# Optimization experiments

Measured on AMD Instinct MI355X. Metric: run time of the kernel, lower is better.

The kernel has to match this reference:

```python
import jax, jax.numpy as jnp
import numpy as np

N_UP, N_DOWN, N_NUC = 16, 16, 4
N_ELEC = N_UP + N_DOWN          # 32
N_ALL = N_ELEC + N_NUC          # 36
BASIS = 32
KDIM = 128                      # kernel_dim
EDIM = 128                      # embedding_dim
HID_K = 64                      # round(sqrt(32*128)) log-spaced hidden of kernel MLP
HID_O = 128                     # round(sqrt(128*128)) hidden of embed_out MLP
N_INT = 3
BATCH = 512
LOG2 = float(np.log(2.0))


def ssp(x):
    # shifted softplus used by SchNet: softplus(x) - log(2)
    return jax.nn.softplus(x) - LOG2


def _conv_indexing(n_elec, n_all):
    # np.mask_indices(n_all, nondiag): all off-diagonal (i, j), row-major
    mask = ~np.eye(n_all, dtype=bool)
    i, j = np.nonzero(mask)
    n = n_elec * (n_all - 1)
    return i[:n], j[:n]


def setup_inputs() -> dict:
    key = jax.random.key(0)
    ks = jax.random.split(key, 16)
    f32 = jnp.float32
    # per-spin shared electron embeddings (torch expand semantics)
    e_up = jax.random.normal(ks[0], (EDIM,), f32)
    e_down = jax.random.normal(ks[1], (EDIM,), f32)
    embedding_elec = jnp.concatenate(
        [jnp.tile(e_up, (N_UP, 1)), jnp.tile(e_down, (N_DOWN, 1))], axis=0
    )  # (N_ELEC, EDIM)
    embedding_nuc = jax.random.normal(ks[2], (N_NUC, KDIM), f32)

    def lin_init(k, out_d, in_d):
        bound = 1.0 / np.sqrt(in_d)
        return jax.random.uniform(k, (out_d, in_d), f32, -bound, bound)

    kk = jax.random.split(ks[3], 9 * N_INT)
    kernel_w1 = jnp.stack([lin_init(kk[9 * t + 0], HID_K, BASIS) for t in range(N_INT)])
    kernel_b1 = jnp.stack([jax.random.uniform(kk[9 * t + 1], (HID_K,), f32, -1, 1) * (1.0 / np.sqrt(BASIS)) for t in range(N_INT)])
    kernel_w2 = jnp.stack([lin_init(kk[9 * t + 2], KDIM, HID_K) for t in range(N_INT)])
    kernel_b2 = jnp.stack([jax.random.uniform(kk[9 * t + 3], (KDIM,), f32, -1, 1) * (1.0 / np.sqrt(HID_K)) for t in range(N_INT)])
    embed_in_w = jnp.stack([lin_init(kk[9 * t + 4], KDIM, EDIM) for t in range(N_INT)])
    embed_out_w1 = jnp.stack([lin_init(kk[9 * t + 5], HID_O, KDIM) for t in range(N_INT)])
    embed_out_b1 = jnp.stack([jax.random.uniform(kk[9 * t + 6], (HID_O,), f32, -1, 1) * (1.0 / np.sqrt(KDIM)) for t in range(N_INT)])
    embed_out_w2 = jnp.stack([lin_init(kk[9 * t + 7], EDIM, HID_O) for t in range(N_INT)])
    embed_out_b2 = jnp.stack([jax.random.uniform(kk[9 * t + 8], (EDIM,), f32, -1, 1) * (1.0 / np.sqrt(HID_O)) for t in range(N_INT)])

    dists_basis = jax.random.normal(ks[4], (BATCH, N_ELEC, N_ALL, BASIS), f32)
    return {
        "dists_basis": dists_basis,
        "embedding_elec": embedding_elec,
        "embedding_nuc": embedding_nuc,
        "kernel_w1": kernel_w1, "kernel_b1": kernel_b1,
        "kernel_w2": kernel_w2, "kernel_b2": kernel_b2,
        "embed_in_w": embed_in_w,
        "embed_out_w1": embed_out_w1, "embed_out_b1": embed_out_b1,
        "embed_out_w2": embed_out_w2, "embed_out_b2": embed_out_b2,
    }


def reference(dists_basis, embedding_elec, embedding_nuc,
              kernel_w1, kernel_b1, kernel_w2, kernel_b2,
              embed_in_w, embed_out_w1, embed_out_b1,
              embed_out_w2, embed_out_b2):
    B, n_elec, n_all, _ = dists_basis.shape
    c_i, c_j = _conv_indexing(n_elec, n_all)  # static numpy index arrays
    db = dists_basis[:, c_i, c_j, :]          # (B, n_pairs, BASIS)

    xs = jnp.broadcast_to(embedding_elec, (B, n_elec, EDIM))
    nuc = jnp.broadcast_to(embedding_nuc, (B, N_NUC, KDIM))
    for t in range(N_INT):
        # pairwise kernel MLP: BASIS -> HID_K -> KDIM with SSP
        h = ssp(jnp.einsum('bpi,hi->bph', db, kernel_w1[t]) + kernel_b1[t])
        Ws = jnp.einsum('bph,kh->bpk', h, kernel_w2[t]) + kernel_b2[t]  # (B,P,K)
        zs = jnp.einsum('bed,kd->bek', xs, embed_in_w[t])               # (B,n_elec,K)
        zs = jnp.concatenate([zs, nuc], axis=1)                         # (B,n_all,K)
        zj = zs[:, c_j]                                                 # (B,P,K)
        z = (Ws.reshape(B, n_elec, n_all - 1, KDIM)
             * zj.reshape(B, n_elec, n_all - 1, KDIM)).sum(axis=2)      # (B,n_elec,K)
        h2 = ssp(jnp.einsum('bek,hk->beh', z, embed_out_w1[t]) + embed_out_b1[t])
        xs = xs + jnp.einsum('beh,dh->bed', h2, embed_out_w2[t]) + embed_out_b2[t]
    return xs
```

## Files before the change

kernel.cpp:

```cpp
#include <hip/hip_runtime.h>
#include <hip/hip_bf16.h>
#include <stdint.h>

#define NBATCH 512
#define NE 32
#define NA 36
#define BAS 32
#define KD 128
#define ED 128
#define HK 64
#define HO 128
#define NT 3

#define XST 132
#define AST 136
#define ZJST 36
#define HB2 44

typedef uint16_t u16;
typedef uint32_t u32;
using bfrag = __attribute__((ext_vector_type(8))) short;
using f32x4 = __attribute__((ext_vector_type(4))) float;
using u32x2 = __attribute__((ext_vector_type(2))) unsigned int;
using u32x4 = __attribute__((ext_vector_type(4))) unsigned int;

#define MFMA(a, b, c) __builtin_amdgcn_mfma_f32_16x16x32_bf16(a, b, c, 0, 0, 0)

__device__ __forceinline__ short ftob(float f) {
    union { __hip_bfloat16 h; short s; } u;
    u.h = __float2bfloat16(f);
    return u.s;
}
__device__ __forceinline__ u32 pk2(float lo, float hi) {
    return ((u32)(u16)ftob(hi) << 16) | (u32)(u16)ftob(lo);
}
__device__ __forceinline__ float bf2f(u16 u) {
    return __uint_as_float(((u32)u) << 16);
}
__device__ __forceinline__ bfrag cvt8(float4 a, float4 c) {
    bfrag r;
    r[0] = ftob(a.x); r[1] = ftob(a.y); r[2] = ftob(a.z); r[3] = ftob(a.w);
    r[4] = ftob(c.x); r[5] = ftob(c.y); r[6] = ftob(c.z); r[7] = ftob(c.w);
    return r;
}
__device__ __forceinline__ bfrag ldf_frag(const float* p) {
    float4 a = *(const float4*)p;
    float4 c = *(const float4*)(p + 4);
    return cvt8(a, c);
}
__device__ __forceinline__ float sspv(float x) {
    return __logf(fmaf(__expf(x), 0.5f, 0.5f));
}

__global__ __launch_bounds__(512, 4) void schnet_mfma(
    const float* __restrict__ db_g,
    const float* __restrict__ ee_g,
    const float* __restrict__ en_g,
    const float* __restrict__ w1_g,
    const float* __restrict__ b1_g,
    const float* __restrict__ w2_g,
    const float* __restrict__ b2_g,
    const float* __restrict__ win_g,
    const float* __restrict__ wo1_g,
    const float* __restrict__ bo1_g,
    const float* __restrict__ wo2_g,
    const float* __restrict__ bo2_g,
    float* __restrict__ out_g)
{
    __shared__ __align__(16) float xs[NE * XST];
    __shared__ __align__(16) u16 xz[NE * AST];
    __shared__ __align__(16) u16 zst[KD * ZJST];
    __shared__ __align__(16) u32 arena32[8 * 16 * HB2];
    __shared__ __align__(16) u16 w2x[8 * 2 * 64 * 8];
    __shared__ __align__(16) u16 w1x[4 * 64 * 8];
    __shared__ __align__(16) float bb2[KD];
    __shared__ __align__(16) float sall[KD];
    __shared__ __align__(16) float bb1[HK];
    u16* h2b = (u16*)arena32;

    const int tid = threadIdx.x;
    const int b = blockIdx.x;
    const int w = tid >> 6;
    const int l = tid & 63;
    const int lm = l & 15;
    const int lq = l >> 4;

    {
        int idx = tid * 8;
        float4 v0 = *(const float4*)(ee_g + idx);
        float4 v1 = *(const float4*)(ee_g + idx + 4);
        int row = idx >> 7, col = idx & 127;
        *(float4*)&xs[row * XST + col] = v0;
        *(float4*)&xs[row * XST + col + 4] = v1;
        *(bfrag*)&xz[row * AST + col] = cvt8(v0, v1);
    }
    {
        int k = tid & 127, rr = tid >> 7;
        zst[k * ZJST + 32 + rr] = (u16)ftob(en_g[rr * 128 + k]);
    }
    __syncthreads();

    for (int t = 0; t < NT; t++) {
#pragma unroll
        for (int uu = 0; uu < 2; uu++) {
            int u = tid + uu * 512;
            int n = u >> 7, s = (u >> 6) & 1, lane = u & 63;
            int lmm = lane & 15, lqq = lane >> 4;
            const float* p = w2_g + (size_t)(t * KD + n * 16 + lmm) * HK + s * 32 + lqq * 8;
            *(bfrag*)&w2x[u * 8] = ldf_frag(p);
        }
        if (tid < 256) {
            int n = tid >> 6, lane = tid & 63;
            const float* p = w1_g + (size_t)(t * HK + n * 16 + (lane & 15)) * BAS
                             + ((lane >> 4) & 3) * 8;
            *(bfrag*)&w1x[tid * 8] = ldf_frag(p);
        } else if (tid < 384) {
            bb2[tid - 256] = b2_g[t * KD + tid - 256];
        } else if (tid < 448) {
            bb1[tid - 384] = b1_g[t * HK + tid - 384];
        }

        {
            bfrag wb[4];
#pragma unroll
            for (int ks = 0; ks < 4; ks++)
                wb[ks] = ldf_frag(win_g + (size_t)(t * KD + w * 16 + lm) * ED + ks * 32 + lq * 8);
            f32x4 c[2];
            c[0] = (f32x4){0.f, 0.f, 0.f, 0.f};
            c[1] = (f32x4){0.f, 0.f, 0.f, 0.f};
#pragma unroll
            for (int m = 0; m < 2; m++)
#pragma unroll
                for (int ks = 0; ks < 4; ks++) {
                    bfrag a = *(const bfrag*)&xz[(m * 16 + lm) * AST + ks * 32 + lq * 8];
                    c[m] = MFMA(a, wb[ks], c[m]);
                }
            u32x2 dd0, dd1;
            dd0.x = pk2(c[0][0], c[0][1]);
            dd0.y = pk2(c[0][2], c[0][3]);
            dd1.x = pk2(c[1][0], c[1][1]);
            dd1.y = pk2(c[1][2], c[1][3]);
            *(u32x2*)&zst[(w * 16 + lm) * ZJST + lq * 4] = dd0;
            *(u32x2*)&zst[(w * 16 + lm) * ZJST + 16 + lq * 4] = dd1;
            float s = __uint_as_float(dd0.x << 16) + __uint_as_float(dd0.x & 0xffff0000u)
                    + __uint_as_float(dd0.y << 16) + __uint_as_float(dd0.y & 0xffff0000u)
                    + __uint_as_float(dd1.x << 16) + __uint_as_float(dd1.x & 0xffff0000u)
                    + __uint_as_float(dd1.y << 16) + __uint_as_float(dd1.y & 0xffff0000u);
            s += __shfl_xor(s, 16, 64);
            s += __shfl_xor(s, 32, 64);
            u32x2 nd = *(const u32x2*)&zst[(w * 16 + lm) * ZJST + 32];
            s += __uint_as_float(nd.x << 16) + __uint_as_float(nd.x & 0xffff0000u)
               + __uint_as_float(nd.y << 16) + __uint_as_float(nd.y & 0xffff0000u);
            if (lq == 0) sall[w * 16 + lm] = s;
        }
        __syncthreads();

        {
            u32* hbw = arena32 + w * (16 * HB2);
            float4 a0, a1, b0, b1;
            const f32x4 zq = (f32x4){0.f, 0.f, 0.f, 0.f};

            auto tile_g12 = [&](bfrag ad, int jc, u32 kmA, u32 kmB, u32 kmC,
                                u32 kmD, float* acc) {
                f32x4 c1[4];
#pragma unroll
                for (int n = 0; n < 4; n++) {
                    f32x4 ci = *(const f32x4*)&bb1[n * 16 + lq * 4];
                    bfrag w1f = *(const bfrag*)&w1x[(n * 64 + l) * 8];
                    c1[n] = MFMA(w1f, ad, ci);
                }
#pragma unroll
                for (int n = 0; n < 4; n++) {
                    u32x2 pp;
                    pp.x = pk2(sspv(c1[n][0]), sspv(c1[n][1]));
                    pp.y = pk2(sspv(c1[n][2]), sspv(c1[n][3]));
                    *(u32x2*)&hbw[lm * HB2 + n * 8 + lq * 2] = pp;
                }
                __builtin_amdgcn_sched_barrier(0);
                union { u32x4 u; bfrag f; } ua, ub;
                ua.u = *(const u32x4*)&hbw[lm * HB2 + lq * 4];
                ub.u = *(const u32x4*)&hbw[lm * HB2 + 16 + lq * 4];
                bfrag a20 = ua.f;
                bfrag a21 = ub.f;
                __builtin_amdgcn_sched_barrier(0);
#pragma unroll
                for (int g = 0; g < 2; g++) {
#pragma unroll
                    for (int nn = 0; nn < 4; nn++) {
                        const int n = g * 4 + nn;
                        bfrag wf0 = *(const bfrag*)&w2x[(n * 128 + l) * 8];
                        bfrag wf1 = *(const bfrag*)&w2x[(n * 128 + 64 + l) * 8];
                        f32x4 c2 = MFMA(a20, wf0, zq);
                        c2 = MFMA(a21, wf1, c2);
                        u32x2 zd = *(const u32x2*)&zst[(n * 16 + lm) * ZJST + jc];
                        acc[n] = fmaf(c2[0], __uint_as_float((zd.x << 16) & kmA), acc[n]);
                        acc[n] = fmaf(c2[1], __uint_as_float(zd.x & kmB), acc[n]);
                        acc[n] = fmaf(c2[2], __uint_as_float((zd.y << 16) & kmC), acc[n]);
                        acc[n] = fmaf(c2[3], __uint_as_float(zd.y & kmD), acc[n]);
                    }
                    __builtin_amdgcn_sched_barrier(0);
                }
            };

            {
                {
                    int e0 = w * 4 + (lm >> 2), j0 = 32 + (lm & 3);
                    const float* p = db_g + ((size_t)(b * NE + e0) * NA + j0) * BAS + lq * 8;
                    a0 = *(const float4*)p;
                    a1 = *(const float4*)(p + 4);
                }
                {
                    const float* p = db_g + ((size_t)(b * NE + w * 4) * NA + lm) * BAS + lq * 8;
                    b0 = *(const float4*)p;
                    b1 = *(const float4*)(p + 4);
                }
                float znuc[8] = {0.f, 0.f, 0.f, 0.f, 0.f, 0.f, 0.f, 0.f};
                tile_g12(cvt8(a0, a1), 32, ~0u, 0xFFFF0000u, ~0u, 0xFFFF0000u, znuc);
                int e0 = w * 4 + lq;
#pragma unroll
                for (int n = 0; n < 8; n += 2) {
                    u32 pk = pk2(znuc[n], znuc[n + 1]);
                    xz[e0 * AST + n * 16 + lm] = (u16)pk;
                    xz[e0 * AST + (n + 1) * 16 + lm] = (u16)(pk >> 16);
                }
            }

#pragma unroll 1
            for (int le = 0; le < 4; le++) {
                const int e = w * 4 + le;
                float zreg[8] = {0.f, 0.f, 0.f, 0.f, 0.f, 0.f, 0.f, 0.f};
                {
                    const float* p = db_g + ((size_t)(b * NE + e) * NA + 16 + lm) * BAS + lq * 8;
                    a0 = *(const float4*)p;
                    a1 = *(const float4*)(p + 4);
                }
                {
                    int lp0 = lq * 4;
                    u32 k0 = (lp0 + 0 == e) ? 0u : ~0u;
                    u32 k1 = (lp0 + 1 == e) ? 0u : ~0u;
                    u32 k2 = (lp0 + 2 == e) ? 0u : ~0u;
                    u32 k3 = (lp0 + 3 == e) ? 0u : ~0u;
                    tile_g12(cvt8(b0, b1), lp0, k0, k1 & 0xFFFF0000u,
                             k2, k3 & 0xFFFF0000u, zreg);
                }
                {
                    int nle = (le < 3) ? le + 1 : 3;
                    const float* p = db_g + ((size_t)(b * NE + w * 4 + nle) * NA + lm) * BAS + lq * 8;
                    b0 = *(const float4*)p;
                    b1 = *(const float4*)(p + 4);
                }
                {
                    int lp0 = 16 + lq * 4;
                    u32 k0 = (lp0 + 0 == e) ? 0u : ~0u;
                    u32 k1 = (lp0 + 1 == e) ? 0u : ~0u;
                    u32 k2 = (lp0 + 2 == e) ? 0u : ~0u;
                    u32 k3 = (lp0 + 3 == e) ? 0u : ~0u;
                    tile_g12(cvt8(a0, a1), lp0, k0, k1 & 0xFFFF0000u,
                             k2, k3 & 0xFFFF0000u, zreg);
                }
#pragma unroll
                for (int n = 0; n < 8; n++) {
                    float v = zreg[n];
                    v += __shfl_xor(v, 16, 64);
                    v += __shfl_xor(v, 32, 64);
                    zreg[n] = v;
                }
                if (lq == le) {
#pragma unroll
                    for (int n = 0; n < 8; n += 2) {
                        int k0 = n * 16 + lm, k1 = (n + 1) * 16 + lm;
                        float o0 = bf2f(xz[e * AST + k0]);
                        float o1 = bf2f(xz[e * AST + k1]);
                        float ze0 = bf2f(zst[k0 * ZJST + e]);
                        float ze1 = bf2f(zst[k1 * ZJST + e]);
                        float t0 = zreg[n] + o0 + bb2[k0] * (sall[k0] - ze0);
                        float t1 = zreg[n + 1] + o1 + bb2[k1] * (sall[k1] - ze1);
                        u32 pk = pk2(t0, t1);
                        xz[e * AST + k0] = (u16)pk;
                        xz[e * AST + k1] = (u16)(pk >> 16);
                    }
                }
            }
        }
        __syncthreads();

        {
            bfrag wb[4];
#pragma unroll
            for (int ks = 0; ks < 4; ks++)
                wb[ks] = ldf_frag(wo1_g + (size_t)(t * HO + w * 16 + lm) * KD + ks * 32 + lq * 8);
            float bo1v = bo1_g[t * HO + w * 16 + lm];
            f32x4 c[2];
            c[0] = (f32x4){bo1v, bo1v, bo1v, bo1v};
            c[1] = (f32x4){bo1v, bo1v, bo1v, bo1v};
#pragma unroll
            for (int m = 0; m < 2; m++)
#pragma unroll
                for (int ks = 0; ks < 4; ks++) {
                    bfrag a = *(const bfrag*)&xz[(m * 16 + lm) * AST + ks * 32 + lq * 8];
                    c[m] = MFMA(a, wb[ks], c[m]);
                }
#pragma unroll
            for (int m = 0; m < 2; m++) {
                u32 p01 = pk2(sspv(c[m][0]), sspv(c[m][1]));
                u32 p23 = pk2(sspv(c[m][2]), sspv(c[m][3]));
                h2b[(m * 16 + lq * 4 + 0) * AST + w * 16 + lm] = (u16)p01;
                h2b[(m * 16 + lq * 4 + 1) * AST + w * 16 + lm] = (u16)(p01 >> 16);
                h2b[(m * 16 + lq * 4 + 2) * AST + w * 16 + lm] = (u16)p23;
                h2b[(m * 16 + lq * 4 + 3) * AST + w * 16 + lm] = (u16)(p23 >> 16);
            }
        }
        __syncthreads();

        {
            bfrag wb[4];
#pragma unroll
            for (int ks = 0; ks < 4; ks++)
                wb[ks] = ldf_frag(wo2_g + (size_t)(t * ED + w * 16 + lm) * HO + ks * 32 + lq * 8);
            float bo2v = bo2_g[t * ED + w * 16 + lm];
            f32x4 c[2];
            c[0] = (f32x4){bo2v, bo2v, bo2v, bo2v};
            c[1] = (f32x4){bo2v, bo2v, bo2v, bo2v};
#pragma unroll
            for (int m = 0; m < 2; m++)
#pragma unroll
                for (int ks = 0; ks < 4; ks++) {
                    bfrag a = *(const bfrag*)&h2b[(m * 16 + lm) * AST + ks * 32 + lq * 8];
                    c[m] = MFMA(a, wb[ks], c[m]);
                }
#pragma unroll
            for (int m = 0; m < 2; m++) {
                float nv[4];
#pragma unroll
                for (int r = 0; r < 4; r++) {
                    int row = m * 16 + lq * 4 + r, col = w * 16 + lm;
                    nv[r] = xs[row * XST + col] + c[m][r];
                    xs[row * XST + col] = nv[r];
                }
                u32 p01 = pk2(nv[0], nv[1]);
                u32 p23 = pk2(nv[2], nv[3]);
                xz[(m * 16 + lq * 4 + 0) * AST + w * 16 + lm] = (u16)p01;
                xz[(m * 16 + lq * 4 + 1) * AST + w * 16 + lm] = (u16)(p01 >> 16);
                xz[(m * 16 + lq * 4 + 2) * AST + w * 16 + lm] = (u16)p23;
                xz[(m * 16 + lq * 4 + 3) * AST + w * 16 + lm] = (u16)(p23 >> 16);
            }
        }
        __syncthreads();
    }

#pragma unroll
    for (int ii = 0; ii < 2; ii++) {
        int idx = (ii * 512 + tid) * 4;
        int row = idx >> 7, col = idx & 127;
        *(float4*)&out_g[(size_t)b * (NE * ED) + idx] = *(const float4*)&xs[row * XST + col];
    }
}

extern "C" void kernel_launch(void* const* d_in, const int* in_sizes, int n_in,
                              void* d_out, int out_size, void* d_ws, size_t ws_size,
                              hipStream_t stream) {
    schnet_mfma<<<NBATCH, 512, 0, stream>>>(
        (const float*)d_in[0], (const float*)d_in[1], (const float*)d_in[2],
        (const float*)d_in[3], (const float*)d_in[4], (const float*)d_in[5],
        (const float*)d_in[6], (const float*)d_in[7], (const float*)d_in[8],
        (const float*)d_in[9], (const float*)d_in[10], (const float*)d_in[11],
        (float*)d_out);
}
```

Baseline: 232.2 us.

## Keep residual xs in registers and store zj table as 32-bit bf16 words

The fp32 residual xs array leaves LDS and lives in per-thread registers, which are loaded from global at the start and written directly to the output at the end. The zj table changes from packed 16-bit bf16 to one bf16 per 32-bit word, which removes shift and mask unpacking in the inner pair loop. Self-exclusion masking is now applied only on tiles that actually contain the diagonal. In exchange the zj table doubles its LDS footprint, register pressure rises, and the final output stores are strided rather than float4.

Measured after the change: 228.9 us. Within noise of the previous version (-1.4%).

```diff
diff --git a/kernel.cpp b/kernel.cpp
--- a/kernel.cpp
+++ b/kernel.cpp
@@ -12,9 +12,8 @@
 #define HO 128
 #define NT 3
 
-#define XST 132
 #define AST 136
-#define ZJST 36
+#define ZJ32 36
 #define HB2 44
 
 typedef uint16_t u16;
@@ -33,6 +32,9 @@
 }
 __device__ __forceinline__ u32 pk2(float lo, float hi) {
     return ((u32)(u16)ftob(hi) << 16) | (u32)(u16)ftob(lo);
+}
+__device__ __forceinline__ u32 fb32(float f) {
+    return ((u32)(u16)ftob(f)) << 16;
 }
 __device__ __forceinline__ float bf2f(u16 u) {
     return __uint_as_float(((u32)u) << 16);
@@ -67,9 +69,8 @@
     const float* __restrict__ bo2_g,
     float* __restrict__ out_g)
 {
-    __shared__ __align__(16) float xs[NE * XST];
     __shared__ __align__(16) u16 xz[NE * AST];
-    __shared__ __align__(16) u16 zst[KD * ZJST];
+    __shared__ __align__(16) u32 zst32[KD * ZJ32];
     __shared__ __align__(16) u32 arena32[8 * 16 * HB2];
     __shared__ __align__(16) u16 w2x[8 * 2 * 64 * 8];
     __shared__ __align__(16) u16 w1x[4 * 64 * 8];
@@ -85,18 +86,23 @@
     const int lm = l & 15;
     const int lq = l >> 4;
 
+    float xr[8];
+#pragma unroll
+    for (int m = 0; m < 2; m++)
+#pragma unroll
+        for (int r = 0; r < 4; r++)
+            xr[m * 4 + r] = ee_g[(m * 16 + lq * 4 + r) * ED + w * 16 + lm];
+
     {
         int idx = tid * 8;
         float4 v0 = *(const float4*)(ee_g + idx);
         float4 v1 = *(const float4*)(ee_g + idx + 4);
         int row = idx >> 7, col = idx & 127;
-        *(float4*)&xs[row * XST + col] = v0;
-        *(float4*)&xs[row * XST + col + 4] = v1;
         *(bfrag*)&xz[row * AST + col] = cvt8(v0, v1);
     }
     {
         int k = tid & 127, rr = tid >> 7;
-        zst[k * ZJST + 32 + rr] = (u16)ftob(en_g[rr * 128 + k]);
+        zst32[k * ZJ32 + 32 + rr] = fb32(en_g[rr * 128 + k]);
     }
     __syncthreads();
 
@@ -135,22 +141,22 @@
                     bfrag a = *(const bfrag*)&xz[(m * 16 + lm) * AST + ks * 32 + lq * 8];
                     c[m] = MFMA(a, wb[ks], c[m]);
                 }
-            u32x2 dd0, dd1;
-            dd0.x = pk2(c[0][0], c[0][1]);
-            dd0.y = pk2(c[0][2], c[0][3]);
-            dd1.x = pk2(c[1][0], c[1][1]);
-            dd1.y = pk2(c[1][2], c[1][3]);
-            *(u32x2*)&zst[(w * 16 + lm) * ZJST + lq * 4] = dd0;
-            *(u32x2*)&zst[(w * 16 + lm) * ZJST + 16 + lq * 4] = dd1;
-            float s = __uint_as_float(dd0.x << 16) + __uint_as_float(dd0.x & 0xffff0000u)
-                    + __uint_as_float(dd0.y << 16) + __uint_as_float(dd0.y & 0xffff0000u)
-                    + __uint_as_float(dd1.x << 16) + __uint_as_float(dd1.x & 0xffff0000u)
-                    + __uint_as_float(dd1.y << 16) + __uint_as_float(dd1.y & 0xffff0000u);
+            u32x4 q0, q1;
+            q0[0] = fb32(c[0][0]); q0[1] = fb32(c[0][1]);
+            q0[2] = fb32(c[0][2]); q0[3] = fb32(c[0][3]);
+            q1[0] = fb32(c[1][0]); q1[1] = fb32(c[1][1]);
+            q1[2] = fb32(c[1][2]); q1[3] = fb32(c[1][3]);
+            *(u32x4*)&zst32[(w * 16 + lm) * ZJ32 + lq * 4] = q0;
+            *(u32x4*)&zst32[(w * 16 + lm) * ZJ32 + 16 + lq * 4] = q1;
+            float s = __uint_as_float(q0[0]) + __uint_as_float(q0[1])
+                    + __uint_as_float(q0[2]) + __uint_as_float(q0[3])
+                    + __uint_as_float(q1[0]) + __uint_as_float(q1[1])
+                    + __uint_as_float(q1[2]) + __uint_as_float(q1[3]);
             s += __shfl_xor(s, 16, 64);
             s += __shfl_xor(s, 32, 64);
-            u32x2 nd = *(const u32x2*)&zst[(w * 16 + lm) * ZJST + 32];
-            s += __uint_as_float(nd.x << 16) + __uint_as_float(nd.x & 0xffff0000u)
-               + __uint_as_float(nd.y << 16) + __uint_as_float(nd.y & 0xffff0000u);
+            u32x4 nd = *(const u32x4*)&zst32[(w * 16 + lm) * ZJ32 + 32];
+            s += __uint_as_float(nd[0]) + __uint_as_float(nd[1])
+               + __uint_as_float(nd[2]) + __uint_as_float(nd[3]);
             if (lq == 0) sall[w * 16 + lm] = s;
         }
         __syncthreads();
@@ -160,8 +166,8 @@
             float4 a0, a1, b0, b1;
             const f32x4 zq = (f32x4){0.f, 0.f, 0.f, 0.f};
 
-            auto tile_g12 = [&](bfrag ad, int jc, u32 kmA, u32 kmB, u32 kmC,
-                                u32 kmD, float* acc) {
+            auto tile_g12 = [&](bfrag ad, int jc, bool dg, u32 m0, u32 m1,
+                                u32 m2, u32 m3, float* acc) {
                 f32x4 c1[4];
 #pragma unroll
                 for (int n = 0; n < 4; n++) {
@@ -192,11 +198,18 @@
                         bfrag wf1 = *(const bfrag*)&w2x[(n * 128 + 64 + l) * 8];
                         f32x4 c2 = MFMA(a20, wf0, zq);
                         c2 = MFMA(a21, wf1, c2);
-                        u32x2 zd = *(const u32x2*)&zst[(n * 16 + lm) * ZJST + jc];
-                        acc[n] = fmaf(c2[0], __uint_as_float((zd.x << 16) & kmA), acc[n]);
-                        acc[n] = fmaf(c2[1], __uint_as_float(zd.x & kmB), acc[n]);
-                        acc[n] = fmaf(c2[2], __uint_as_float((zd.y << 16) & kmC), acc[n]);
-                        acc[n] = fmaf(c2[3], __uint_as_float(zd.y & kmD), acc[n]);
+                        u32x4 zd = *(const u32x4*)&zst32[(n * 16 + lm) * ZJ32 + jc];
+                        if (dg) {
+                            acc[n] = fmaf(c2[0], __uint_as_float(zd[0] & m0), acc[n]);
+                            acc[n] = fmaf(c2[1], __uint_as_float(zd[1] & m1), acc[n]);
+                            acc[n] = fmaf(c2[2], __uint_as_float(zd[2] & m2), acc[n]);
+                            acc[n] = fmaf(c2[3], __uint_as_float(zd[3] & m3), acc[n]);
+                        } else {
+                            acc[n] = fmaf(c2[0], __uint_as_float(zd[0]), acc[n]);
+                            acc[n] = fmaf(c2[1], __uint_as_float(zd[1]), acc[n]);
+                            acc[n] = fmaf(c2[2], __uint_as_float(zd[2]), acc[n]);
+                            acc[n] = fmaf(c2[3], __uint_as_float(zd[3]), acc[n]);
+                        }
                     }
                     __builtin_amdgcn_sched_barrier(0);
                 }
@@ -215,7 +228,7 @@
                     b1 = *(const float4*)(p + 4);
                 }
                 float znuc[8] = {0.f, 0.f, 0.f, 0.f, 0.f, 0.f, 0.f, 0.f};
-                tile_g12(cvt8(a0, a1), 32, ~0u, 0xFFFF0000u, ~0u, 0xFFFF0000u, znuc);
+                tile_g12(cvt8(a0, a1), 32, false, 0u, 0u, 0u, 0u, znuc);
                 int e0 = w * 4 + lq;
 #pragma unroll
                 for (int n = 0; n < 8; n += 2) {
@@ -236,12 +249,11 @@
                 }
                 {
                     int lp0 = lq * 4;
-                    u32 k0 = (lp0 + 0 == e) ? 0u : ~0u;
-                    u32 k1 = (lp0 + 1 == e) ? 0u : ~0u;
-                    u32 k2 = (lp0 + 2 == e) ? 0u : ~0u;
-                    u32 k3 = (lp0 + 3 == e) ? 0u : ~0u;
-                    tile_g12(cvt8(b0, b1), lp0, k0, k1 & 0xFFFF0000u,
-                             k2, k3 & 0xFFFF0000u, zreg);
+                    u32 m0 = (lp0 + 0 == e) ? 0u : ~0u;
+                    u32 m1 = (lp0 + 1 == e) ? 0u : ~0u;
+                    u32 m2 = (lp0 + 2 == e) ? 0u : ~0u;
+                    u32 m3 = (lp0 + 3 == e) ? 0u : ~0u;
+                    tile_g12(cvt8(b0, b1), lp0, e < 16, m0, m1, m2, m3, zreg);
                 }
                 {
                     int nle = (le < 3) ? le + 1 : 3;
@@ -251,12 +263,11 @@
                 }
                 {
                     int lp0 = 16 + lq * 4;
-                    u32 k0 = (lp0 + 0 == e) ? 0u : ~0u;
-                    u32 k1 = (lp0 + 1 == e) ? 0u : ~0u;
-                    u32 k2 = (lp0 + 2 == e) ? 0u : ~0u;
-                    u32 k3 = (lp0 + 3 == e) ? 0u : ~0u;
-                    tile_g12(cvt8(a0, a1), lp0, k0, k1 & 0xFFFF0000u,
-                             k2, k3 & 0xFFFF0000u, zreg);
+                    u32 m0 = (lp0 + 0 == e) ? 0u : ~0u;
+                    u32 m1 = (lp0 + 1 == e) ? 0u : ~0u;
+                    u32 m2 = (lp0 + 2 == e) ? 0u : ~0u;
+                    u32 m3 = (lp0 + 3 == e) ? 0u : ~0u;
+                    tile_g12(cvt8(a0, a1), lp0, e >= 16, m0, m1, m2, m3, zreg);
                 }
 #pragma unroll
                 for (int n = 0; n < 8; n++) {
@@ -271,8 +282,8 @@
                         int k0 = n * 16 + lm, k1 = (n + 1) * 16 + lm;
                         float o0 = bf2f(xz[e * AST + k0]);
                         float o1 = bf2f(xz[e * AST + k1]);
-                        float ze0 = bf2f(zst[k0 * ZJST + e]);
-                        float ze1 = bf2f(zst[k1 * ZJST + e]);
+                        float ze0 = __uint_as_float(zst32[k0 * ZJ32 + e]);
+                        float ze1 = __uint_as_float(zst32[k1 * ZJ32 + e]);
                         float t0 = zreg[n] + o0 + bb2[k0] * (sall[k0] - ze0);
                         float t1 = zreg[n + 1] + o1 + bb2[k1] * (sall[k1] - ze1);
                         u32 pk = pk2(t0, t1);
@@ -330,15 +341,11 @@
                 }
 #pragma unroll
             for (int m = 0; m < 2; m++) {
-                float nv[4];
-#pragma unroll
-                for (int r = 0; r < 4; r++) {
-                    int row = m * 16 + lq * 4 + r, col = w * 16 + lm;
-                    nv[r] = xs[row * XST + col] + c[m][r];
-                    xs[row * XST + col] = nv[r];
-                }
-                u32 p01 = pk2(nv[0], nv[1]);
-                u32 p23 = pk2(nv[2], nv[3]);
+#pragma unroll
+                for (int r = 0; r < 4; r++)
+                    xr[m * 4 + r] += c[m][r];
+                u32 p01 = pk2(xr[m * 4 + 0], xr[m * 4 + 1]);
+                u32 p23 = pk2(xr[m * 4 + 2], xr[m * 4 + 3]);
                 xz[(m * 16 + lq * 4 + 0) * AST + w * 16 + lm] = (u16)p01;
                 xz[(m * 16 + lq * 4 + 1) * AST + w * 16 + lm] = (u16)(p01 >> 16);
                 xz[(m * 16 + lq * 4 + 2) * AST + w * 16 + lm] = (u16)p23;
@@ -349,11 +356,11 @@
     }
 
 #pragma unroll
-    for (int ii = 0; ii < 2; ii++) {
-        int idx = (ii * 512 + tid) * 4;
-        int row = idx >> 7, col = idx & 127;
-        *(float4*)&out_g[(size_t)b * (NE * ED) + idx] = *(const float4*)&xs[row * XST + col];
-    }
+    for (int m = 0; m < 2; m++)
+#pragma unroll
+        for (int r = 0; r < 4; r++)
+            out_g[(size_t)b * (NE * ED) + (m * 16 + lq * 4 + r) * ED + w * 16 + lm] =
+                xr[m * 4 + r];
 }
 
 extern "C" void kernel_launch(void* const* d_in, const int* in_sizes, int n_in,
```
